# Performance work log

Hardware: AMD Instinct MI355X
Metric: run time of the kernel (lower is better)

The kernel has to match this reference:

```python
import jax, jax.numpy as jnp
import numpy as np

B, LQ, LK = 4, 2048, 2048
DQ, DK, DO = 1024, 1024, 1024


def setup_inputs() -> dict:
    key = jax.random.key(0)
    ks = jax.random.split(key, 9)
    s = 0.02
    return {
        "query_input": jax.random.normal(ks[0], (B, LQ, DQ), jnp.float32),
        "key_input": jax.random.normal(ks[1], (B, LK, DK), jnp.float32),
        "value_input": jax.random.normal(ks[2], (B, LK, DK), jnp.float32),
        "Wq": jax.random.normal(ks[3], (DQ, DO), jnp.float32) * s,
        "bq": jax.random.normal(ks[4], (DO,), jnp.float32) * s,
        "Wk": jax.random.normal(ks[5], (DK, DO), jnp.float32) * s,
        "bk": jax.random.normal(ks[6], (DO,), jnp.float32) * s,
        "Wv": jax.random.normal(ks[7], (DK, DO), jnp.float32) * s,
        "bv": jax.random.normal(ks[8], (DO,), jnp.float32) * s,
    }


def reference(query_input, key_input, value_input, Wq, bq, Wk, bk, Wv, bv):
    scale = jnp.asarray(DO, query_input.dtype) ** 0.5
    q = query_input @ Wq + bq              # [B, Lq, D]
    k = key_input @ Wk + bk                # [B, Lk, D]
    v = value_input @ Wv + bv              # [B, Lk, D]
    attn = jnp.einsum("bqd,bkd->bqk", q, k) / scale
    attn = jax.nn.softmax(attn, axis=-1)
    return jnp.einsum("bqk,bkd->bqd", attn, v)
```

## Files before the change

kernel.cpp:

```cpp
#include <hip/hip_runtime.h>

typedef _Float16 f16x8 __attribute__((ext_vector_type(8)));
typedef _Float16 f16x4 __attribute__((ext_vector_type(4)));
typedef float f32x4 __attribute__((ext_vector_type(4)));
typedef int   v4i   __attribute__((ext_vector_type(4)));

__device__ __forceinline__ void lds_load16(const _Float16* g, _Float16* l) {
    __builtin_amdgcn_global_load_lds(
        (const __attribute__((address_space(1))) void*)g,
        (__attribute__((address_space(3))) void*)l,
        16, 0, 0);
}

__device__ __forceinline__ f16x8 ldsr(unsigned a) {
    v4i r;
    asm volatile("ds_read_b128 %0, %1" : "=v"(r) : "v"(a));
    return __builtin_bit_cast(f16x8, r);
}

template <int MODE>
__global__ __launch_bounds__(512, 2)
void gemm_core(const _Float16* A0, const _Float16* B0, void* C0, const float* b0,
               const _Float16* A1, const _Float16* B1, void* C1, const float* b1,
               const _Float16* A2, const _Float16* B2, void* C2, const float* b2,
               float* rowsum)
{
    constexpr int BM  = (MODE == 5) ? 128 : 256;
    constexpr int K   = (MODE == 5) ? 2048 : 1024;
    constexpr int LDA = (MODE == 5) ? 2048 : 1024;
    constexpr int LDB = (MODE == 5) ? 8192 : 1024;
    constexpr int NT  = K / 64;
    constexpr int MI  = BM / 32;
    constexpr int MH  = MI / 2;
    constexpr int LA  = BM / 64;

    __shared__ __align__(16) _Float16 As[2][BM * 64];
    __shared__ __align__(16) _Float16 Bs[2][256 * 64];

    const int z_ = blockIdx.z;
    const int bx = blockIdx.x, by = blockIdx.y;
    const int t    = threadIdx.x;
    const int w    = t >> 6;
    const int lane = t & 63;
    const int ln   = lane & 15;
    const int kq   = lane >> 4;
    const int wm   = (w >> 2) * (BM / 2);
    const int wn   = (w & 3) * 64;

    const _Float16* A;
    const _Float16* B;
    size_t cbase = 0;
    int m0, n0, z = z_;

    if (MODE == 0) {
        A = z == 0 ? A0 : z == 1 ? A1 : A2;
        B = z == 0 ? B0 : z == 1 ? B1 : B2;
        if (z == 2) { m0 = (by & 3) * 256;             n0 = (bx * 4 + (by >> 2)) * 256; }
        else        { m0 = (bx * 4 + (by >> 2)) * 256; n0 = (by & 3) * 256; }
    } else if (MODE == 3) {
        A = A0 + (size_t)z * 2048 * 1024;
        B = B0 + (size_t)z * 2048 * 1024;
        cbase = (size_t)z * 2048 * 2048;
        rowsum += z * 2048;
        m0 = ((bx & 3) * 2 + (by >> 2)) * 256;
        n0 = ((bx >> 2) * 4 + (by & 3)) * 256;
    } else {
        z = (blockIdx.z << 1) | (bx >> 2);
        A = A0 + (size_t)z * 2048 * 2048;
        B = B0 + (size_t)z * 2048;
        cbase = (size_t)z * 2048 * 1024;
        rowsum += z * 2048;
        m0 = by * 128;
        n0 = (bx & 3) * 256;
    }

    const int r6 = t >> 3;
    const int cw = ((t & 7) ^ (r6 & 7)) * 8;
    const _Float16* gA = A + (size_t)(m0 + r6) * LDA + cw;
    const _Float16* gB = B + (size_t)(n0 + r6) * LDB + cw;

    auto stage = [&](int b, int kt) {
#pragma unroll
        for (int s = 0; s < LA; ++s)
            lds_load16(gA + (size_t)(s * 64) * LDA + kt * 64, As[b] + s * 4096 + w * 512);
#pragma unroll
        for (int s = 0; s < 4; ++s)
            lds_load16(gB + (size_t)(s * 64) * LDB + kt * 64, Bs[b] + s * 4096 + w * 512);
    };

    const int xr  = ln & 7;
    const int sk0 = ((0 + kq) ^ xr) * 8;
    const int sk1 = ((4 + kq) ^ xr) * 8;
    const int ra  = (wm + ln) * 64;
    const int rb  = (wn + ln) * 64;

    const unsigned uA0 = (unsigned)(uintptr_t)(__attribute__((address_space(3))) _Float16*)&As[0][0];
    const unsigned uA1 = (unsigned)(uintptr_t)(__attribute__((address_space(3))) _Float16*)&As[1][0];
    const unsigned uB0 = (unsigned)(uintptr_t)(__attribute__((address_space(3))) _Float16*)&Bs[0][0];
    const unsigned uB1 = (unsigned)(uintptr_t)(__attribute__((address_space(3))) _Float16*)&Bs[1][0];
    const unsigned aA[2][2] = { { uA0 + 2u * (ra + sk0), uA0 + 2u * (ra + sk1) },
                                { uA1 + 2u * (ra + sk0), uA1 + 2u * (ra + sk1) } };
    const unsigned aB[2][2] = { { uB0 + 2u * (rb + sk0), uB0 + 2u * (rb + sk1) },
                                { uB1 + 2u * (rb + sk0), uB1 + 2u * (rb + sk1) } };

    f16x8 af[MH][2], bf[4][2];
    f32x4 acc[MI][4] = {};

    stage(0, 0);
    stage(1, 1);
    if constexpr (MODE == 5) asm volatile("s_waitcnt vmcnt(6)" ::: "memory");
    else                     asm volatile("s_waitcnt vmcnt(8)" ::: "memory");
    __builtin_amdgcn_s_barrier();
    __builtin_amdgcn_sched_barrier(0);

#pragma unroll 2
    for (int kc = 0; kc < NT; ++kc) {
        const int b = kc & 1;

#pragma unroll
        for (int i = 0; i < MH; ++i) {
            af[i][0] = ldsr(aA[b][0] + i * 2048);
            af[i][1] = ldsr(aA[b][1] + i * 2048);
        }
#pragma unroll
        for (int j = 0; j < 2; ++j) {
            bf[j][0] = ldsr(aB[b][0] + j * 2048);
            bf[j][1] = ldsr(aB[b][1] + j * 2048);
        }
        __builtin_amdgcn_s_barrier();
        asm volatile("s_waitcnt lgkmcnt(0)" ::: "memory");
        __builtin_amdgcn_sched_barrier(0);
        __builtin_amdgcn_s_setprio(1);
#pragma unroll
        for (int i = 0; i < MH; ++i)
#pragma unroll
            for (int j = 0; j < 2; ++j) {
                acc[i][j] = __builtin_amdgcn_mfma_f32_16x16x32_f16(af[i][0], bf[j][0], acc[i][j], 0, 0, 0);
                acc[i][j] = __builtin_amdgcn_mfma_f32_16x16x32_f16(af[i][1], bf[j][1], acc[i][j], 0, 0, 0);
            }
        __builtin_amdgcn_s_setprio(0);
        __builtin_amdgcn_s_barrier();
        __builtin_amdgcn_sched_barrier(0);

#pragma unroll
        for (int j = 2; j < 4; ++j) {
            bf[j][0] = ldsr(aB[b][0] + j * 2048);
            bf[j][1] = ldsr(aB[b][1] + j * 2048);
        }
        __builtin_amdgcn_s_barrier();
        asm volatile("s_waitcnt lgkmcnt(0)" ::: "memory");
        __builtin_amdgcn_sched_barrier(0);
        __builtin_amdgcn_s_setprio(1);
#pragma unroll
        for (int i = 0; i < MH; ++i)
#pragma unroll
            for (int j = 2; j < 4; ++j) {
                acc[i][j] = __builtin_amdgcn_mfma_f32_16x16x32_f16(af[i][0], bf[j][0], acc[i][j], 0, 0, 0);
                acc[i][j] = __builtin_amdgcn_mfma_f32_16x16x32_f16(af[i][1], bf[j][1], acc[i][j], 0, 0, 0);
            }
        __builtin_amdgcn_s_setprio(0);
        __builtin_amdgcn_s_barrier();
        __builtin_amdgcn_sched_barrier(0);

#pragma unroll
        for (int i = 0; i < MH; ++i) {
            af[i][0] = ldsr(aA[b][0] + (i + MH) * 2048);
            af[i][1] = ldsr(aA[b][1] + (i + MH) * 2048);
        }
        __builtin_amdgcn_s_barrier();
        asm volatile("s_waitcnt lgkmcnt(0)" ::: "memory");
        __builtin_amdgcn_sched_barrier(0);
        __builtin_amdgcn_s_setprio(1);
#pragma unroll
        for (int i = 0; i < MH; ++i)
#pragma unroll
            for (int j = 0; j < 2; ++j) {
                acc[i + MH][j] = __builtin_amdgcn_mfma_f32_16x16x32_f16(af[i][0], bf[j][0], acc[i + MH][j], 0, 0, 0);
                acc[i + MH][j] = __builtin_amdgcn_mfma_f32_16x16x32_f16(af[i][1], bf[j][1], acc[i + MH][j], 0, 0, 0);
            }
        __builtin_amdgcn_s_setprio(0);
        __builtin_amdgcn_s_barrier();
        __builtin_amdgcn_sched_barrier(0);

        if (kc + 2 < NT) {
            stage(b, kc + 2);
            if constexpr (MODE == 5) asm volatile("s_waitcnt vmcnt(6)" ::: "memory");
            else                     asm volatile("s_waitcnt vmcnt(8)" ::: "memory");
        } else if (kc + 1 < NT) {
            asm volatile("s_waitcnt vmcnt(0)" ::: "memory");
        }
        __builtin_amdgcn_s_barrier();
        __builtin_amdgcn_sched_barrier(0);
        __builtin_amdgcn_s_setprio(1);
#pragma unroll
        for (int i = 0; i < MH; ++i)
#pragma unroll
            for (int j = 2; j < 4; ++j) {
                acc[i + MH][j] = __builtin_amdgcn_mfma_f32_16x16x32_f16(af[i][0], bf[j][0], acc[i + MH][j], 0, 0, 0);
                acc[i + MH][j] = __builtin_amdgcn_mfma_f32_16x16x32_f16(af[i][1], bf[j][1], acc[i + MH][j], 0, 0, 0);
            }
        __builtin_amdgcn_s_setprio(0);
        __builtin_amdgcn_s_barrier();
        __builtin_amdgcn_sched_barrier(0);
    }

    if (MODE == 0) {
        _Float16* Cp = (_Float16*)(z == 0 ? C0 : z == 1 ? C1 : C2);
        const float* bp = z == 0 ? b0 : z == 1 ? b1 : b2;
        const int ldc = (z == 2) ? 8192 : 1024;
#pragma unroll
        for (int i = 0; i < MI; ++i) {
            const int rbase = m0 + wm + i * 16 + kq * 4;
#pragma unroll
            for (int j = 0; j < 4; ++j) {
                const int gcol = n0 + wn + j * 16 + ln;
#pragma unroll
                for (int r = 0; r < 4; ++r) {
                    float vv = acc[i][j][r] + (z == 2 ? bp[rbase + r] : bp[gcol]);
                    Cp[(size_t)(rbase + r) * ldc + gcol] = (_Float16)vv;
                }
            }
        }
    } else if (MODE == 3) {
        _Float16* Ch = (_Float16*)C0;
#pragma unroll
        for (int i = 0; i < MI; ++i) {
            const int rbase = m0 + wm + i * 16 + kq * 4;
            float rs[4] = {0.f, 0.f, 0.f, 0.f};
#pragma unroll
            for (int j = 0; j < 4; ++j) {
                const int gcol = n0 + wn + j * 16 + ln;
#pragma unroll
                for (int r = 0; r < 4; ++r) {
                    float e = __expf(acc[i][j][r] * 0.03125f);
                    Ch[cbase + (size_t)(rbase + r) * 2048 + gcol] = (_Float16)e;
                    rs[r] += e;
                }
            }
#pragma unroll
            for (int r = 0; r < 4; ++r) {
                float s = rs[r];
                s += __shfl_xor(s, 1);
                s += __shfl_xor(s, 2);
                s += __shfl_xor(s, 4);
                s += __shfl_xor(s, 8);
                if (ln == 0) atomicAdd(&rowsum[rbase + r], s);
            }
        }
    } else {
        float* Cf = (float*)C0;
#pragma unroll
        for (int i = 0; i < MI; ++i) {
            const int rbase = m0 + wm + i * 16 + kq * 4;
            float inv[4];
#pragma unroll
            for (int r = 0; r < 4; ++r) inv[r] = 1.f / rowsum[rbase + r];
#pragma unroll
            for (int j = 0; j < 4; ++j) {
                const int gcol = n0 + wn + j * 16 + ln;
#pragma unroll
                for (int r = 0; r < 4; ++r)
                    Cf[cbase + (size_t)(rbase + r) * 1024 + gcol] = acc[i][j][r] * inv[r];
            }
        }
    }
}

__global__ __launch_bounds__(256)
void prep(const float4* __restrict__ x0, _Float16* __restrict__ y0,
          const float4* __restrict__ x1, _Float16* __restrict__ y1,
          const float4* __restrict__ x2, _Float16* __restrict__ y2,
          const float* __restrict__ W0, _Float16* __restrict__ T0,
          const float* __restrict__ W1, _Float16* __restrict__ T1,
          const float* __restrict__ W2, _Float16* __restrict__ T2,
          float* __restrict__ rowsum)
{
    if (blockIdx.y < 3) {
        const size_t i = (size_t)blockIdx.x * 256 + threadIdx.x;
        const float4* x = blockIdx.y == 0 ? x0 : blockIdx.y == 1 ? x1 : x2;
        _Float16*    yy = blockIdx.y == 0 ? y0 : blockIdx.y == 1 ? y1 : y2;
        float4 f = x[i];
        f16x4 o = { (_Float16)f.x, (_Float16)f.y, (_Float16)f.z, (_Float16)f.w };
        *(f16x4*)(yy + i * 4) = o;
        if (blockIdx.y == 0 && blockIdx.x < 32)
            rowsum[blockIdx.x * 256 + threadIdx.x] = 0.f;
        return;
    }
    if (blockIdx.x >= 3072) return;
    const int zz = blockIdx.x >> 10;
    const int tb = blockIdx.x & 1023;
    const float* W = zz == 0 ? W0 : zz == 1 ? W1 : W2;
    _Float16*   WT = zz == 0 ? T0 : zz == 1 ? T1 : T2;
    __shared__ float tile[32][33];
    const int bxs = (tb & 31) * 32;
    const int bys = (tb >> 5) * 32;
    const int tx = threadIdx.x & 31;
    const int ty = threadIdx.x >> 5;
#pragma unroll
    for (int i = ty; i < 32; i += 8)
        tile[i][tx] = W[(size_t)(bys + i) * 1024 + bxs + tx];
    __syncthreads();
#pragma unroll
    for (int i = ty; i < 32; i += 8)
        WT[(size_t)(bxs + i) * 1024 + bys + tx] = (_Float16)tile[tx][i];
}

extern "C" void kernel_launch(void* const* d_in, const int* in_sizes, int n_in,
                              void* d_out, int out_size, void* d_ws, size_t ws_size,
                              hipStream_t stream)
{
    const float* Xq = (const float*)d_in[0];
    const float* Xk = (const float*)d_in[1];
    const float* Xv = (const float*)d_in[2];
    const float* Wq = (const float*)d_in[3];
    const float* bq = (const float*)d_in[4];
    const float* Wk = (const float*)d_in[5];
    const float* bk = (const float*)d_in[6];
    const float* Wv = (const float*)d_in[7];
    const float* bv = (const float*)d_in[8];
    float* out = (float*)d_out;

    const size_t XN = (size_t)8192 * 1024;
    const size_t WN = (size_t)1024 * 1024;

    _Float16* ws  = (_Float16*)d_ws;
    _Float16* Xqh = ws;
    _Float16* Xkh = Xqh + XN;
    _Float16* Xvh = Xkh + XN;
    _Float16* WqT = Xvh + XN;
    _Float16* WkT = WqT + WN;
    _Float16* WvT = WkT + WN;
    _Float16* qh  = WvT + WN;
    _Float16* kh  = qh + XN;
    _Float16* vT  = kh + XN;
    _Float16* S   = vT + XN;
    float* rowsum = (float*)(S + (size_t)4 * 2048 * 2048);

    {
        dim3 g(8192, 4);
        prep<<<g, 256, 0, stream>>>((const float4*)Xq, Xqh,
                                    (const float4*)Xk, Xkh,
                                    (const float4*)Xv, Xvh,
                                    Wq, WqT, Wk, WkT, Wv, WvT, rowsum);
    }

    {
        dim3 g(8, 16, 3);
        gemm_core<0><<<g, 512, 0, stream>>>(
            Xqh, WqT, qh, bq,
            Xkh, WkT, kh, bk,
            WvT, Xvh, vT, bv,
            nullptr);
    }

    {
        dim3 g(8, 8, 4);
        gemm_core<3><<<g, 512, 0, stream>>>(
            qh, kh, S, nullptr,
            nullptr, nullptr, nullptr, nullptr,
            nullptr, nullptr, nullptr, nullptr,
            rowsum);
    }

    {
        dim3 g(8, 16, 2);
        gemm_core<5><<<g, 512, 0, stream>>>(
            S, vT, out, nullptr,
            nullptr, nullptr, nullptr, nullptr,
            nullptr, nullptr, nullptr, nullptr,
            rowsum);
    }
}
```

Measured before the change: 313.2 us.

## Spread LDS prefetch across MFMA phases and reorder MFMAs by k-half

Breaks the single end-of-iteration global-to-LDS prefetch into pieces issued across the four compute phases. Each piece targets a region of the shared tile that has already been consumed into registers, so memory traffic overlaps more of the MFMA work. Also reorders the MFMA loops so the k-half index is outermost, which places independent accumulator updates back to back instead of chaining dependent ones. The risk is extra scheduling pressure and ordering hazards in the LDS buffers, although the split appears to respect which buffer regions have already been read.

```diff
diff --git a/kernel.cpp b/kernel.cpp
--- a/kernel.cpp
+++ b/kernel.cpp
@@ -33,6 +33,7 @@
     constexpr int MI  = BM / 32;
     constexpr int MH  = MI / 2;
     constexpr int LA  = BM / 64;
+    constexpr int LT  = LA + 4;
 
     __shared__ __align__(16) _Float16 As[2][BM * 64];
     __shared__ __align__(16) _Float16 Bs[2][256 * 64];
@@ -79,13 +80,11 @@
     const _Float16* gA = A + (size_t)(m0 + r6) * LDA + cw;
     const _Float16* gB = B + (size_t)(n0 + r6) * LDB + cw;
 
-    auto stage = [&](int b, int kt) {
-#pragma unroll
-        for (int s = 0; s < LA; ++s)
-            lds_load16(gA + (size_t)(s * 64) * LDA + kt * 64, As[b] + s * 4096 + w * 512);
-#pragma unroll
-        for (int s = 0; s < 4; ++s)
-            lds_load16(gB + (size_t)(s * 64) * LDB + kt * 64, Bs[b] + s * 4096 + w * 512);
+    auto stA = [&](int b, int kt, int s) {
+        lds_load16(gA + (size_t)(s * 64) * LDA + kt * 64, As[b] + s * 4096 + w * 512);
+    };
+    auto stB = [&](int b, int kt, int s) {
+        lds_load16(gB + (size_t)(s * 64) * LDB + kt * 64, Bs[b] + s * 4096 + w * 512);
     };
 
     const int xr  = ln & 7;
@@ -106,8 +105,16 @@
     f16x8 af[MH][2], bf[4][2];
     f32x4 acc[MI][4] = {};
 
-    stage(0, 0);
-    stage(1, 1);
+    {
+#pragma unroll
+        for (int s = 0; s < LA; ++s) stA(0, 0, s);
+#pragma unroll
+        for (int s = 0; s < 4; ++s)  stB(0, 0, s);
+#pragma unroll
+        for (int s = 0; s < LA; ++s) stA(1, 1, s);
+#pragma unroll
+        for (int s = 0; s < 4; ++s)  stB(1, 1, s);
+    }
     if constexpr (MODE == 5) asm volatile("s_waitcnt vmcnt(6)" ::: "memory");
     else                     asm volatile("s_waitcnt vmcnt(8)" ::: "memory");
     __builtin_amdgcn_s_barrier();
@@ -115,7 +122,8 @@
 
 #pragma unroll 2
     for (int kc = 0; kc < NT; ++kc) {
-        const int b = kc & 1;
+        const int  b  = kc & 1;
+        const bool pf = (kc + 2 < NT);
 
 #pragma unroll
         for (int i = 0; i < MH; ++i) {
@@ -132,12 +140,12 @@
         __builtin_amdgcn_sched_barrier(0);
         __builtin_amdgcn_s_setprio(1);
 #pragma unroll
-        for (int i = 0; i < MH; ++i)
-#pragma unroll
-            for (int j = 0; j < 2; ++j) {
-                acc[i][j] = __builtin_amdgcn_mfma_f32_16x16x32_f16(af[i][0], bf[j][0], acc[i][j], 0, 0, 0);
-                acc[i][j] = __builtin_amdgcn_mfma_f32_16x16x32_f16(af[i][1], bf[j][1], acc[i][j], 0, 0, 0);
-            }
+        for (int kh = 0; kh < 2; ++kh)
+#pragma unroll
+            for (int i = 0; i < MH; ++i)
+#pragma unroll
+                for (int j = 0; j < 2; ++j)
+                    acc[i][j] = __builtin_amdgcn_mfma_f32_16x16x32_f16(af[i][kh], bf[j][kh], acc[i][j], 0, 0, 0);
         __builtin_amdgcn_s_setprio(0);
         __builtin_amdgcn_s_barrier();
         __builtin_amdgcn_sched_barrier(0);
@@ -147,17 +155,20 @@
             bf[j][0] = ldsr(aB[b][0] + j * 2048);
             bf[j][1] = ldsr(aB[b][1] + j * 2048);
         }
+        if constexpr (LA == 4) {
+            if (pf) { stA(b, kc + 2, 0); stA(b, kc + 2, 2); }
+        }
         __builtin_amdgcn_s_barrier();
         asm volatile("s_waitcnt lgkmcnt(0)" ::: "memory");
         __builtin_amdgcn_sched_barrier(0);
         __builtin_amdgcn_s_setprio(1);
 #pragma unroll
-        for (int i = 0; i < MH; ++i)
-#pragma unroll
-            for (int j = 2; j < 4; ++j) {
-                acc[i][j] = __builtin_amdgcn_mfma_f32_16x16x32_f16(af[i][0], bf[j][0], acc[i][j], 0, 0, 0);
-                acc[i][j] = __builtin_amdgcn_mfma_f32_16x16x32_f16(af[i][1], bf[j][1], acc[i][j], 0, 0, 0);
-            }
+        for (int kh = 0; kh < 2; ++kh)
+#pragma unroll
+            for (int i = 0; i < MH; ++i)
+#pragma unroll
+                for (int j = 2; j < 4; ++j)
+                    acc[i][j] = __builtin_amdgcn_mfma_f32_16x16x32_f16(af[i][kh], bf[j][kh], acc[i][j], 0, 0, 0);
         __builtin_amdgcn_s_setprio(0);
         __builtin_amdgcn_s_barrier();
         __builtin_amdgcn_sched_barrier(0);
@@ -167,23 +178,26 @@
             af[i][0] = ldsr(aA[b][0] + (i + MH) * 2048);
             af[i][1] = ldsr(aA[b][1] + (i + MH) * 2048);
         }
+        if (pf) { stB(b, kc + 2, 0); stB(b, kc + 2, 1); stB(b, kc + 2, 2); }
         __builtin_amdgcn_s_barrier();
         asm volatile("s_waitcnt lgkmcnt(0)" ::: "memory");
         __builtin_amdgcn_sched_barrier(0);
         __builtin_amdgcn_s_setprio(1);
 #pragma unroll
-        for (int i = 0; i < MH; ++i)
-#pragma unroll
-            for (int j = 0; j < 2; ++j) {
-                acc[i + MH][j] = __builtin_amdgcn_mfma_f32_16x16x32_f16(af[i][0], bf[j][0], acc[i + MH][j], 0, 0, 0);
-                acc[i + MH][j] = __builtin_amdgcn_mfma_f32_16x16x32_f16(af[i][1], bf[j][1], acc[i + MH][j], 0, 0, 0);
-            }
+        for (int kh = 0; kh < 2; ++kh)
+#pragma unroll
+            for (int i = 0; i < MH; ++i)
+#pragma unroll
+                for (int j = 0; j < 2; ++j)
+                    acc[i + MH][j] = __builtin_amdgcn_mfma_f32_16x16x32_f16(af[i][kh], bf[j][kh], acc[i + MH][j], 0, 0, 0);
         __builtin_amdgcn_s_setprio(0);
         __builtin_amdgcn_s_barrier();
         __builtin_amdgcn_sched_barrier(0);
 
-        if (kc + 2 < NT) {
-            stage(b, kc + 2);
+        if (pf) {
+            stB(b, kc + 2, 3);
+            if constexpr (LA == 4) { stA(b, kc + 2, 1); stA(b, kc + 2, 3); }
+            else                   { stA(b, kc + 2, 0); stA(b, kc + 2, 1); }
             if constexpr (MODE == 5) asm volatile("s_waitcnt vmcnt(6)" ::: "memory");
             else                     asm volatile("s_waitcnt vmcnt(8)" ::: "memory");
         } else if (kc + 1 < NT) {
@@ -193,12 +207,12 @@
         __builtin_amdgcn_sched_barrier(0);
         __builtin_amdgcn_s_setprio(1);
 #pragma unroll
-        for (int i = 0; i < MH; ++i)
-#pragma unroll
-            for (int j = 2; j < 4; ++j) {
-                acc[i + MH][j] = __builtin_amdgcn_mfma_f32_16x16x32_f16(af[i][0], bf[j][0], acc[i + MH][j], 0, 0, 0);
-                acc[i + MH][j] = __builtin_amdgcn_mfma_f32_16x16x32_f16(af[i][1], bf[j][1], acc[i + MH][j], 0, 0, 0);
-            }
+        for (int kh = 0; kh < 2; ++kh)
+#pragma unroll
+            for (int i = 0; i < MH; ++i)
+#pragma unroll
+                for (int j = 2; j < 4; ++j)
+                    acc[i + MH][j] = __builtin_amdgcn_mfma_f32_16x16x32_f16(af[i][kh], bf[j][kh], acc[i + MH][j], 0, 0, 0);
         __builtin_amdgcn_s_setprio(0);
         __builtin_amdgcn_s_barrier();
         __builtin_amdgcn_sched_barrier(0);
```

Measured after the change: 305.3 us. -2.5%, faster.
